# Kernel tuning notes

Hardware: AMD Instinct MI355X
Metric: run time of the kernel (lower is better)

Reference implementation:

```python
import jax, jax.numpy as jnp
import numpy as np


def setup_inputs() -> dict:
    key = jax.random.key(0)
    k_x, k_w, k_W, k_b, k_idx = jax.random.split(key, 5)
    B, C, N, K, O = 2, 32, 40962, 25, 64
    x = jax.random.normal(k_x, (B, C, N), dtype=jnp.float32)
    neigh_weights = jax.random.uniform(k_w, (N, K, 3), dtype=jnp.float32)
    W = jax.random.normal(k_W, (O, K * C), dtype=jnp.float32) * 0.02
    b = jax.random.normal(k_b, (O,), dtype=jnp.float32) * 0.02
    neigh_indices = jax.random.randint(k_idx, (N, K, 3), 0, N, dtype=jnp.int32)
    return {"x": x, "neigh_weights": neigh_weights, "W": W, "b": b,
            "neigh_indices": neigh_indices}


def reference(x, neigh_weights, W, b, neigh_indices):
    # x: (B, C, N); neigh_indices/neigh_weights: (N, K, 3); W: (O, C*K); b: (O,)
    B, C, N = x.shape
    _, K, _ = neigh_indices.shape
    # Gather neighbor features: (B, C, N, K, 3)
    mat = x[:, :, neigh_indices]
    # Barycentric weighted sum over the 3 triangle vertices -> (B, C, N, K)
    s = jnp.einsum('bcnkt,nkt->bcnk', mat, neigh_weights)
    # Permute to (B, N, C, K) and apply Linear(C*K -> O)
    feat = s.transpose(0, 2, 1, 3).reshape(B * N, C * K)
    out = feat @ W.T + b  # (B*N, O)
    out = out.reshape(B, N, -1).transpose(0, 2, 1)  # (B, O, N)
    return out
```

## Files before the change

kernel.cpp:

```cpp
#include <hip/hip_runtime.h>
#include <hip/hip_fp16.h>

typedef __attribute__((ext_vector_type(8))) _Float16 half8;
typedef __attribute__((ext_vector_type(4))) float f32x4;

union U2H2 { unsigned int u; __half2 h; };

static __device__ __forceinline__ unsigned int pack2h(float a, float b) {
    U2H2 c; c.h = __floats2half2_rn(a, b); return c.u;
}
static __device__ __forceinline__ __half2 u_as_h2(unsigned int u) {
    U2H2 c; c.u = u; return c.h;
}

#define SWZ(row, slot) ((slot) ^ ((row) & 3) ^ (((row) >> 2) & 3))

#define LDS_BARRIER()                                                \
    do {                                                             \
        asm volatile("s_waitcnt lgkmcnt(0)" ::: "memory");           \
        __builtin_amdgcn_s_barrier();                                \
        __builtin_amdgcn_sched_barrier(0);                           \
    } while (0)

__global__ void prep_w(const float* __restrict__ W, unsigned short* __restrict__ Wrh) {
    int i = blockIdx.x * 256 + threadIdx.x;
    if (i >= 25 * 2048) return;
    int c = i & 31, o = (i >> 5) & 63, k = i >> 11;
    __half h = __float2half(W[o * 800 + c * 25 + k]);
    Wrh[i] = *reinterpret_cast<unsigned short*>(&h);
}

__global__ __launch_bounds__(256) void transpose_x(const float* __restrict__ x,
                                                   unsigned short* __restrict__ xth, int N) {
    __shared__ float t[2][32][65];
    int n0 = blockIdx.x * 64, tid = threadIdx.x;
#pragma unroll
    for (int i = 0; i < 16; ++i) {
        int e = tid + 256 * i;
        int b = e >> 11, c = (e >> 6) & 31, nl = e & 63;
        int n = n0 + nl;
        t[b][c][nl] = (n < N) ? x[(size_t)(b * 32 + c) * N + n] : 0.f;
    }
    __syncthreads();
    int nl = tid >> 2, q = tid & 3, n = n0 + nl;
    if (n < N) {
#pragma unroll
        for (int b = 0; b < 2; ++b) {
            uint4 p;
            p.x = pack2h(t[b][q * 8 + 0][nl], t[b][q * 8 + 1][nl]);
            p.y = pack2h(t[b][q * 8 + 2][nl], t[b][q * 8 + 3][nl]);
            p.z = pack2h(t[b][q * 8 + 4][nl], t[b][q * 8 + 5][nl]);
            p.w = pack2h(t[b][q * 8 + 6][nl], t[b][q * 8 + 7][nl]);
            *reinterpret_cast<uint4*>(xth + ((size_t)n * 64 + b * 32 + q * 8)) = p;
        }
    }
}

__global__ __launch_bounds__(256) void fused_main(
    const unsigned short* __restrict__ xth,
    const unsigned short* __restrict__ Wrh,
    const float* __restrict__ bias,
    const int* __restrict__ nidx,
    const float* __restrict__ nw,
    float* __restrict__ out,
    int N)
{
    __shared__ unsigned int idxw[25 * 96];
    __shared__ __align__(16) unsigned char sA[2][4096];
    __shared__ __align__(16) unsigned char sB[2][4096];

    const int tid = threadIdx.x;
    const int n0 = blockIdx.x * 32;

#pragma unroll
    for (int it = 0; it < 10; ++it) {
        int e = tid + 256 * it;
        if (e < 2400) {
            int nl = e / 75;
            int rem = e - nl * 75;
            int n = n0 + nl;
            unsigned int u = 0;
            if (n < N) {
                int j = nidx[(size_t)n0 * 75 + e];
                __half hw = __float2half(nw[(size_t)n0 * 75 + e]);
                u = (unsigned int)j |
                    ((unsigned int)*reinterpret_cast<unsigned short*>(&hw) << 16);
            }
            int kk = rem / 3, t = rem - kk * 3;
            idxw[(kk * 32 + nl) * 3 + t] = u;
        }
    }
    __syncthreads();

    const int row = tid >> 2;
    const int l4  = tid & 3;
    const int b0  = row >> 5;
    const int nl0 = row & 31;

    const int wr_off = row * 64 + (SWZ(row, l4) << 4);
    const int sb_off = wr_off;

    const int l = tid & 63, wv = tid >> 6, c16 = l & 15, g = l >> 4;
    const int arow = 16 * wv + c16;
    const int rd_a = arow * 64 + (SWZ(arow, g) << 4);

    unsigned int ru[2][3];
    uint4 rg[2][3];
    uint4 rB;

    auto issue_g = [&](int kk, int buf) {
        const unsigned int* ip = &idxw[(kk * 32 + nl0) * 3];
#pragma unroll
        for (int t = 0; t < 3; ++t) {
            unsigned int u = ip[t];
            if (buf == 0) ru[0][t] = u; else ru[1][t] = u;
            uint4 v = *reinterpret_cast<const uint4*>(
                xth + ((size_t)(u & 0xffffu) * 64 + b0 * 32 + l4 * 8));
            if (buf == 0) rg[0][t] = v; else rg[1][t] = v;
        }
    };

    f32x4 acc[4];
#pragma unroll
    for (int ot = 0; ot < 4; ++ot) acc[ot] = (f32x4){0.f, 0.f, 0.f, 0.f};

    rB = *reinterpret_cast<const uint4*>(Wrh + tid * 8);
    issue_g(0, 0);
    issue_g(1, 1);

#pragma unroll 2
    for (int k = 0; k < 25; ++k) {
        const int buf = k & 1;

        *reinterpret_cast<uint4*>(&sB[buf][sb_off]) = rB;
        {
            int kB = (k + 1 < 25) ? k + 1 : 24;
            rB = *reinterpret_cast<const uint4*>(Wrh + kB * 2048 + tid * 8);
        }

        {
            unsigned int u0, u1, u2;
            uint4 v0, v1, v2;
            if (buf == 0) { u0 = ru[0][0]; u1 = ru[0][1]; u2 = ru[0][2];
                            v0 = rg[0][0]; v1 = rg[0][1]; v2 = rg[0][2]; }
            else          { u0 = ru[1][0]; u1 = ru[1][1]; u2 = ru[1][2];
                            v0 = rg[1][0]; v1 = rg[1][1]; v2 = rg[1][2]; }
            __half2 w0 = u_as_h2(__builtin_amdgcn_perm(u0, u0, 0x03020302u));
            __half2 w1 = u_as_h2(__builtin_amdgcn_perm(u1, u1, 0x03020302u));
            __half2 w2 = u_as_h2(__builtin_amdgcn_perm(u2, u2, 0x03020302u));
            uint4 p; U2H2 c;
            c.h = __hfma2(u_as_h2(v0.x), w0, __hfma2(u_as_h2(v1.x), w1, __hmul2(u_as_h2(v2.x), w2)));
            p.x = c.u;
            c.h = __hfma2(u_as_h2(v0.y), w0, __hfma2(u_as_h2(v1.y), w1, __hmul2(u_as_h2(v2.y), w2)));
            p.y = c.u;
            c.h = __hfma2(u_as_h2(v0.z), w0, __hfma2(u_as_h2(v1.z), w1, __hmul2(u_as_h2(v2.z), w2)));
            p.z = c.u;
            c.h = __hfma2(u_as_h2(v0.w), w0, __hfma2(u_as_h2(v1.w), w1, __hmul2(u_as_h2(v2.w), w2)));
            p.w = c.u;
            *reinterpret_cast<uint4*>(&sA[buf][wr_off]) = p;
        }
        {
            int kg = (k + 2 < 25) ? k + 2 : 24;
            issue_g(kg, buf);
        }

        LDS_BARRIER();

        {
            half8 af = *reinterpret_cast<const half8*>(&sA[buf][rd_a]);
#pragma unroll
            for (int ot = 0; ot < 4; ++ot) {
                int orow = ot * 16 + c16;
                half8 bf = *reinterpret_cast<const half8*>(
                    &sB[buf][orow * 64 + (SWZ(orow, g) << 4)]);
                acc[ot] = __builtin_amdgcn_mfma_f32_16x16x32_f16(af, bf, acc[ot], 0, 0, 0);
            }
        }
    }

#pragma unroll
    for (int ot = 0; ot < 4; ++ot) {
        int o = ot * 16 + c16;
        float bv = bias[o];
#pragma unroll
        for (int i = 0; i < 4; ++i) {
            int mrow = 16 * wv + 4 * g + i;
            int b = mrow >> 5, nl = mrow & 31;
            int n = n0 + nl;
            if (n < N) out[(size_t)(b * 64 + o) * N + n] = acc[ot][i] + bv;
        }
    }
}

extern "C" void kernel_launch(void* const* d_in, const int* in_sizes, int n_in,
                              void* d_out, int out_size, void* d_ws, size_t ws_size,
                              hipStream_t stream) {
    const float* x    = (const float*)d_in[0];
    const float* nw   = (const float*)d_in[1];
    const float* W    = (const float*)d_in[2];
    const float* bias = (const float*)d_in[3];
    const int*   nidx = (const int*)d_in[4];
    float* out = (float*)d_out;

    int N = in_sizes[0] / 64;

    unsigned short* xth = (unsigned short*)d_ws;
    unsigned short* Wrh = xth + (size_t)N * 64;

    prep_w<<<(25 * 2048 + 255) / 256, 256, 0, stream>>>(W, Wrh);

    transpose_x<<<(N + 63) / 64, 256, 0, stream>>>(x, xth, N);

    fused_main<<<(N + 31) / 32, 256, 0, stream>>>(xth, Wrh, bias, nidx, nw, out, N);
}
```

Before: 65.34 us.

## Feed MFMA operands directly from registers, removing LDS staging and barriers

Weights are pre-permuted into the MFMA B-fragment layout so each lane loads its own B operands straight from global memory. Each lane now gathers and blends the A fragment it needs itself, so the shared-memory sA/sB buffers and the per-iteration barrier go away. The loop is unrolled into explicit A/B register double buffers, with setprio around the MFMAs and a launch-bounds occupancy hint. The cost is more global B loads per lane (four instead of one, served by cache) and higher register pressure.

```diff
diff --git a/kernel.cpp b/kernel.cpp
--- a/kernel.cpp
+++ b/kernel.cpp
@@ -13,19 +13,16 @@
     U2H2 c; c.u = u; return c.h;
 }
 
-#define SWZ(row, slot) ((slot) ^ ((row) & 3) ^ (((row) >> 2) & 3))
-
-#define LDS_BARRIER()                                                \
-    do {                                                             \
-        asm volatile("s_waitcnt lgkmcnt(0)" ::: "memory");           \
-        __builtin_amdgcn_s_barrier();                                \
-        __builtin_amdgcn_sched_barrier(0);                           \
-    } while (0)
-
 __global__ void prep_w(const float* __restrict__ W, unsigned short* __restrict__ Wrh) {
     int i = blockIdx.x * 256 + threadIdx.x;
     if (i >= 25 * 2048) return;
-    int c = i & 31, o = (i >> 5) & 63, k = i >> 11;
+    int k = i >> 11;
+    int r = i & 2047;
+    int ot = r >> 9;
+    int l = (r >> 3) & 63;
+    int e = i & 7;
+    int o = ot * 16 + (l & 15);
+    int c = (l >> 4) * 8 + e;
     __half h = __float2half(W[o * 800 + c * 25 + k]);
     Wrh[i] = *reinterpret_cast<unsigned short*>(&h);
 }
@@ -56,7 +53,7 @@
     }
 }
 
-__global__ __launch_bounds__(256) void fused_main(
+__global__ __launch_bounds__(256, 4) void fused_main(
     const unsigned short* __restrict__ xth,
     const unsigned short* __restrict__ Wrh,
     const float* __restrict__ bias,
@@ -66,8 +63,6 @@
     int N)
 {
     __shared__ unsigned int idxw[25 * 96];
-    __shared__ __align__(16) unsigned char sA[2][4096];
-    __shared__ __align__(16) unsigned char sB[2][4096];
 
     const int tid = threadIdx.x;
     const int n0 = blockIdx.x * 32;
@@ -92,91 +87,75 @@
     }
     __syncthreads();
 
-    const int row = tid >> 2;
-    const int l4  = tid & 3;
-    const int b0  = row >> 5;
-    const int nl0 = row & 31;
+    const int wv = tid >> 6, l = tid & 63;
+    const int c16 = l & 15, g = l >> 4;
+    const int row = 16 * wv + c16;
+    const int b0 = row >> 5, nl0 = row & 31;
+    const int xoff = b0 * 32 + g * 8;
 
-    const int wr_off = row * 64 + (SWZ(row, l4) << 4);
-    const int sb_off = wr_off;
+    uint4 rgA[3], rgB[3], rBA[4], rBB[4];
+    unsigned int ruA[3], ruB[3];
 
-    const int l = tid & 63, wv = tid >> 6, c16 = l & 15, g = l >> 4;
-    const int arow = 16 * wv + c16;
-    const int rd_a = arow * 64 + (SWZ(arow, g) << 4);
-
-    unsigned int ru[2][3];
-    uint4 rg[2][3];
-    uint4 rB;
-
-    auto issue_g = [&](int kk, int buf) {
+    auto issue_g = [&](int kk, uint4 (&rg)[3], unsigned int (&ru)[3]) {
         const unsigned int* ip = &idxw[(kk * 32 + nl0) * 3];
 #pragma unroll
         for (int t = 0; t < 3; ++t) {
             unsigned int u = ip[t];
-            if (buf == 0) ru[0][t] = u; else ru[1][t] = u;
-            uint4 v = *reinterpret_cast<const uint4*>(
-                xth + ((size_t)(u & 0xffffu) * 64 + b0 * 32 + l4 * 8));
-            if (buf == 0) rg[0][t] = v; else rg[1][t] = v;
+            ru[t] = u;
+            rg[t] = *reinterpret_cast<const uint4*>(
+                xth + (int)(u & 0xffffu) * 64 + xoff);
         }
+    };
+    auto issue_B = [&](int kk, uint4 (&rB)[4]) {
+        const unsigned short* bp = Wrh + kk * 2048 + l * 8;
+#pragma unroll
+        for (int ot = 0; ot < 4; ++ot)
+            rB[ot] = *reinterpret_cast<const uint4*>(bp + ot * 512);
     };
 
     f32x4 acc[4];
 #pragma unroll
     for (int ot = 0; ot < 4; ++ot) acc[ot] = (f32x4){0.f, 0.f, 0.f, 0.f};
 
-    rB = *reinterpret_cast<const uint4*>(Wrh + tid * 8);
-    issue_g(0, 0);
-    issue_g(1, 1);
+    issue_g(0, rgA, ruA); issue_B(0, rBA);
+    issue_g(1, rgB, ruB); issue_B(1, rBB);
 
-#pragma unroll 2
-    for (int k = 0; k < 25; ++k) {
-        const int buf = k & 1;
+    auto body = [&](int kNext, uint4 (&rg)[3], unsigned int (&ru)[3], uint4 (&rB)[4]) {
+        __half2 w0 = u_as_h2(__builtin_amdgcn_perm(ru[0], ru[0], 0x03020302u));
+        __half2 w1 = u_as_h2(__builtin_amdgcn_perm(ru[1], ru[1], 0x03020302u));
+        __half2 w2 = u_as_h2(__builtin_amdgcn_perm(ru[2], ru[2], 0x03020302u));
+        uint4 v0 = rg[0], v1 = rg[1], v2 = rg[2];
+        uint4 p; U2H2 c;
+        c.h = __hfma2(u_as_h2(v0.x), w0, __hfma2(u_as_h2(v1.x), w1, __hmul2(u_as_h2(v2.x), w2)));
+        p.x = c.u;
+        c.h = __hfma2(u_as_h2(v0.y), w0, __hfma2(u_as_h2(v1.y), w1, __hmul2(u_as_h2(v2.y), w2)));
+        p.y = c.u;
+        c.h = __hfma2(u_as_h2(v0.z), w0, __hfma2(u_as_h2(v1.z), w1, __hmul2(u_as_h2(v2.z), w2)));
+        p.z = c.u;
+        c.h = __hfma2(u_as_h2(v0.w), w0, __hfma2(u_as_h2(v1.w), w1, __hmul2(u_as_h2(v2.w), w2)));
+        p.w = c.u;
+        half8 af = __builtin_bit_cast(half8, p);
 
-        *reinterpret_cast<uint4*>(&sB[buf][sb_off]) = rB;
-        {
-            int kB = (k + 1 < 25) ? k + 1 : 24;
-            rB = *reinterpret_cast<const uint4*>(Wrh + kB * 2048 + tid * 8);
+        issue_g(kNext, rg, ru);
+
+        __builtin_amdgcn_s_setprio(1);
+#pragma unroll
+        for (int ot = 0; ot < 4; ++ot) {
+            half8 bf = __builtin_bit_cast(half8, rB[ot]);
+            acc[ot] = __builtin_amdgcn_mfma_f32_16x16x32_f16(af, bf, acc[ot], 0, 0, 0);
         }
+        __builtin_amdgcn_s_setprio(0);
 
-        {
-            unsigned int u0, u1, u2;
-            uint4 v0, v1, v2;
-            if (buf == 0) { u0 = ru[0][0]; u1 = ru[0][1]; u2 = ru[0][2];
-                            v0 = rg[0][0]; v1 = rg[0][1]; v2 = rg[0][2]; }
-            else          { u0 = ru[1][0]; u1 = ru[1][1]; u2 = ru[1][2];
-                            v0 = rg[1][0]; v1 = rg[1][1]; v2 = rg[1][2]; }
-            __half2 w0 = u_as_h2(__builtin_amdgcn_perm(u0, u0, 0x03020302u));
-            __half2 w1 = u_as_h2(__builtin_amdgcn_perm(u1, u1, 0x03020302u));
-            __half2 w2 = u_as_h2(__builtin_amdgcn_perm(u2, u2, 0x03020302u));
-            uint4 p; U2H2 c;
-            c.h = __hfma2(u_as_h2(v0.x), w0, __hfma2(u_as_h2(v1.x), w1, __hmul2(u_as_h2(v2.x), w2)));
-            p.x = c.u;
-            c.h = __hfma2(u_as_h2(v0.y), w0, __hfma2(u_as_h2(v1.y), w1, __hmul2(u_as_h2(v2.y), w2)));
-            p.y = c.u;
-            c.h = __hfma2(u_as_h2(v0.z), w0, __hfma2(u_as_h2(v1.z), w1, __hmul2(u_as_h2(v2.z), w2)));
-            p.z = c.u;
-            c.h = __hfma2(u_as_h2(v0.w), w0, __hfma2(u_as_h2(v1.w), w1, __hmul2(u_as_h2(v2.w), w2)));
-            p.w = c.u;
-            *reinterpret_cast<uint4*>(&sA[buf][wr_off]) = p;
-        }
-        {
-            int kg = (k + 2 < 25) ? k + 2 : 24;
-            issue_g(kg, buf);
-        }
+        issue_B(kNext, rB);
+    };
 
-        LDS_BARRIER();
-
-        {
-            half8 af = *reinterpret_cast<const half8*>(&sA[buf][rd_a]);
-#pragma unroll
-            for (int ot = 0; ot < 4; ++ot) {
-                int orow = ot * 16 + c16;
-                half8 bf = *reinterpret_cast<const half8*>(
-                    &sB[buf][orow * 64 + (SWZ(orow, g) << 4)]);
-                acc[ot] = __builtin_amdgcn_mfma_f32_16x16x32_f16(af, bf, acc[ot], 0, 0, 0);
-            }
-        }
+    for (int kp = 0; kp < 12; ++kp) {
+        int kE = 2 * kp + 2;
+        int kO = (2 * kp + 3 <= 24) ? 2 * kp + 3 : 24;
+        body(kE, rgA, ruA, rBA);
+        body(kO, rgB, ruB, rBB);
     }
+    body(24, rgA, ruA, rBA);
 
 #pragma unroll
     for (int ot = 0; ot < 4; ++ot) {
```

Result: slower. 94.14 us (+44.1%).

## Deepen gather prefetch to four stages, merge prep kernels, simplify index staging

Applied to the files above, without the earlier changes.

Merges the weight-conversion and x-transpose prep kernels into one launch, with extra blocks handling the W conversion, which removes one kernel launch. In the main kernel, the neighbor-feature gather prefetch goes from two steps ahead to four, using four explicit register sets and a manually unrolled K loop, to hide more gather latency. The index/weight staging now stores in natural order (row*75), so the div/mod remapping goes away, and gather addressing uses 32-bit arithmetic. The trade-off is more live registers, which may reduce occupancy.

```diff
diff --git a/kernel.cpp b/kernel.cpp
--- a/kernel.cpp
+++ b/kernel.cpp
@@ -22,18 +22,25 @@
         __builtin_amdgcn_sched_barrier(0);                           \
     } while (0)
 
-__global__ void prep_w(const float* __restrict__ W, unsigned short* __restrict__ Wrh) {
-    int i = blockIdx.x * 256 + threadIdx.x;
-    if (i >= 25 * 2048) return;
-    int c = i & 31, o = (i >> 5) & 63, k = i >> 11;
-    __half h = __float2half(W[o * 800 + c * 25 + k]);
-    Wrh[i] = *reinterpret_cast<unsigned short*>(&h);
-}
-
-__global__ __launch_bounds__(256) void transpose_x(const float* __restrict__ x,
-                                                   unsigned short* __restrict__ xth, int N) {
+__global__ __launch_bounds__(256) void prep_all(const float* __restrict__ x,
+                                                const float* __restrict__ W,
+                                                unsigned short* __restrict__ xth,
+                                                unsigned short* __restrict__ Wrh,
+                                                int N, int nT) {
+    int bid = blockIdx.x, tid = threadIdx.x;
+    if (bid >= nT) {
+        int k = bid - nT;
+#pragma unroll
+        for (int it = 0; it < 8; ++it) {
+            int r = tid + 256 * it;
+            int o = r >> 5, c = r & 31;
+            __half h = __float2half(W[o * 800 + c * 25 + k]);
+            Wrh[k * 2048 + r] = *reinterpret_cast<unsigned short*>(&h);
+        }
+        return;
+    }
     __shared__ float t[2][32][65];
-    int n0 = blockIdx.x * 64, tid = threadIdx.x;
+    int n0 = bid * 64;
 #pragma unroll
     for (int i = 0; i < 16; ++i) {
         int e = tid + 256 * i;
@@ -65,7 +72,7 @@
     float* __restrict__ out,
     int N)
 {
-    __shared__ unsigned int idxw[25 * 96];
+    __shared__ unsigned int idxw[32 * 75];
     __shared__ __align__(16) unsigned char sA[2][4096];
     __shared__ __align__(16) unsigned char sB[2][4096];
 
@@ -76,9 +83,7 @@
     for (int it = 0; it < 10; ++it) {
         int e = tid + 256 * it;
         if (e < 2400) {
-            int nl = e / 75;
-            int rem = e - nl * 75;
-            int n = n0 + nl;
+            int n = n0 + e / 75;
             unsigned int u = 0;
             if (n < N) {
                 int j = nidx[(size_t)n0 * 75 + e];
@@ -86,8 +91,7 @@
                 u = (unsigned int)j |
                     ((unsigned int)*reinterpret_cast<unsigned short*>(&hw) << 16);
             }
-            int kk = rem / 3, t = rem - kk * 3;
-            idxw[(kk * 32 + nl) * 3 + t] = u;
+            idxw[e] = u;
         }
     }
     __syncthreads();
@@ -98,85 +102,92 @@
     const int nl0 = row & 31;
 
     const int wr_off = row * 64 + (SWZ(row, l4) << 4);
-    const int sb_off = wr_off;
 
     const int l = tid & 63, wv = tid >> 6, c16 = l & 15, g = l >> 4;
     const int arow = 16 * wv + c16;
     const int rd_a = arow * 64 + (SWZ(arow, g) << 4);
 
-    unsigned int ru[2][3];
-    uint4 rg[2][3];
+    uint4 rg0[3], rg1[3], rg2[3], rg3[3];
+    unsigned int ru0[3], ru1[3], ru2[3], ru3[3];
     uint4 rB;
 
-    auto issue_g = [&](int kk, int buf) {
-        const unsigned int* ip = &idxw[(kk * 32 + nl0) * 3];
-#pragma unroll
-        for (int t = 0; t < 3; ++t) {
-            unsigned int u = ip[t];
-            if (buf == 0) ru[0][t] = u; else ru[1][t] = u;
-            uint4 v = *reinterpret_cast<const uint4*>(
-                xth + ((size_t)(u & 0xffffu) * 64 + b0 * 32 + l4 * 8));
-            if (buf == 0) rg[0][t] = v; else rg[1][t] = v;
-        }
-    };
+    const unsigned int* iprow = &idxw[nl0 * 75];
+
+#define ISSUE_G(kk, RG, RU)                                                     \
+    do {                                                                        \
+        _Pragma("unroll")                                                       \
+        for (int t = 0; t < 3; ++t) {                                           \
+            unsigned int u = iprow[(kk) * 3 + t];                               \
+            RU[t] = u;                                                          \
+            RG[t] = *reinterpret_cast<const uint4*>(                            \
+                xth + (int)(u & 0xffffu) * 64 + b0 * 32 + l4 * 8);              \
+        }                                                                       \
+    } while (0)
 
     f32x4 acc[4];
 #pragma unroll
     for (int ot = 0; ot < 4; ++ot) acc[ot] = (f32x4){0.f, 0.f, 0.f, 0.f};
 
     rB = *reinterpret_cast<const uint4*>(Wrh + tid * 8);
-    issue_g(0, 0);
-    issue_g(1, 1);
-
-#pragma unroll 2
-    for (int k = 0; k < 25; ++k) {
-        const int buf = k & 1;
-
-        *reinterpret_cast<uint4*>(&sB[buf][sb_off]) = rB;
-        {
-            int kB = (k + 1 < 25) ? k + 1 : 24;
-            rB = *reinterpret_cast<const uint4*>(Wrh + kB * 2048 + tid * 8);
-        }
-
-        {
-            unsigned int u0, u1, u2;
-            uint4 v0, v1, v2;
-            if (buf == 0) { u0 = ru[0][0]; u1 = ru[0][1]; u2 = ru[0][2];
-                            v0 = rg[0][0]; v1 = rg[0][1]; v2 = rg[0][2]; }
-            else          { u0 = ru[1][0]; u1 = ru[1][1]; u2 = ru[1][2];
-                            v0 = rg[1][0]; v1 = rg[1][1]; v2 = rg[1][2]; }
-            __half2 w0 = u_as_h2(__builtin_amdgcn_perm(u0, u0, 0x03020302u));
-            __half2 w1 = u_as_h2(__builtin_amdgcn_perm(u1, u1, 0x03020302u));
-            __half2 w2 = u_as_h2(__builtin_amdgcn_perm(u2, u2, 0x03020302u));
-            uint4 p; U2H2 c;
-            c.h = __hfma2(u_as_h2(v0.x), w0, __hfma2(u_as_h2(v1.x), w1, __hmul2(u_as_h2(v2.x), w2)));
-            p.x = c.u;
-            c.h = __hfma2(u_as_h2(v0.y), w0, __hfma2(u_as_h2(v1.y), w1, __hmul2(u_as_h2(v2.y), w2)));
-            p.y = c.u;
-            c.h = __hfma2(u_as_h2(v0.z), w0, __hfma2(u_as_h2(v1.z), w1, __hmul2(u_as_h2(v2.z), w2)));
-            p.z = c.u;
-            c.h = __hfma2(u_as_h2(v0.w), w0, __hfma2(u_as_h2(v1.w), w1, __hmul2(u_as_h2(v2.w), w2)));
-            p.w = c.u;
-            *reinterpret_cast<uint4*>(&sA[buf][wr_off]) = p;
-        }
-        {
-            int kg = (k + 2 < 25) ? k + 2 : 24;
-            issue_g(kg, buf);
-        }
-
-        LDS_BARRIER();
-
-        {
-            half8 af = *reinterpret_cast<const half8*>(&sA[buf][rd_a]);
-#pragma unroll
-            for (int ot = 0; ot < 4; ++ot) {
-                int orow = ot * 16 + c16;
-                half8 bf = *reinterpret_cast<const half8*>(
-                    &sB[buf][orow * 64 + (SWZ(orow, g) << 4)]);
-                acc[ot] = __builtin_amdgcn_mfma_f32_16x16x32_f16(af, bf, acc[ot], 0, 0, 0);
-            }
-        }
-    }
+    ISSUE_G(0, rg0, ru0);
+    ISSUE_G(1, rg1, ru1);
+    ISSUE_G(2, rg2, ru2);
+    ISSUE_G(3, rg3, ru3);
+
+#define BODY(K, BUF, RG, RU)                                                       \
+    do {                                                                           \
+        const int k_ = (K);                                                        \
+                                              \
+        *reinterpret_cast<uint4*>(&sB[BUF][wr_off]) = rB;                          \
+        if (k_ + 1 < 25)                                                           \
+            rB = *reinterpret_cast<const uint4*>(Wrh + (k_ + 1) * 2048 + tid * 8); \
+                                   \
+        {                                                                          \
+            __half2 w0 = u_as_h2(__builtin_amdgcn_perm(RU[0], RU[0], 0x03020302u));\
+            __half2 w1 = u_as_h2(__builtin_amdgcn_perm(RU[1], RU[1], 0x03020302u));\
+            __half2 w2 = u_as_h2(__builtin_amdgcn_perm(RU[2], RU[2], 0x03020302u));\
+            uint4 v0 = RG[0], v1 = RG[1], v2 = RG[2];                              \
+            uint4 p; U2H2 c;                                                       \
+            c.h = __hfma2(u_as_h2(v0.x), w0,                                       \
+                  __hfma2(u_as_h2(v1.x), w1, __hmul2(u_as_h2(v2.x), w2)));         \
+            p.x = c.u;                                                             \
+            c.h = __hfma2(u_as_h2(v0.y), w0,                                       \
+                  __hfma2(u_as_h2(v1.y), w1, __hmul2(u_as_h2(v2.y), w2)));         \
+            p.y = c.u;                                                             \
+            c.h = __hfma2(u_as_h2(v0.z), w0,                                       \
+                  __hfma2(u_as_h2(v1.z), w1, __hmul2(u_as_h2(v2.z), w2)));         \
+            p.z = c.u;                                                             \
+            c.h = __hfma2(u_as_h2(v0.w), w0,                                       \
+                  __hfma2(u_as_h2(v1.w), w1, __hmul2(u_as_h2(v2.w), w2)));         \
+            p.w = c.u;                                                             \
+            *reinterpret_cast<uint4*>(&sA[BUF][wr_off]) = p;                       \
+        }                                                                          \
+                                     \
+        if (k_ + 4 < 25) ISSUE_G(k_ + 4, RG, RU);                                  \
+                      \
+        LDS_BARRIER();                                                             \
+                                                                \
+        {                                                                          \
+            half8 af = *reinterpret_cast<const half8*>(&sA[BUF][rd_a]);            \
+            _Pragma("unroll")                                                      \
+            for (int ot = 0; ot < 4; ++ot) {                                       \
+                int orow = ot * 16 + c16;                                          \
+                half8 bf = *reinterpret_cast<const half8*>(                        \
+                    &sB[BUF][orow * 64 + (SWZ(orow, g) << 4)]);                    \
+                acc[ot] =                                                          \
+                    __builtin_amdgcn_mfma_f32_16x16x32_f16(af, bf, acc[ot], 0, 0, 0);\
+            }                                                                      \
+        }                                                                          \
+    } while (0)
+
+    for (int kp = 0; kp < 6; ++kp) {
+        int k0 = kp * 4;
+        BODY(k0 + 0, 0, rg0, ru0);
+        BODY(k0 + 1, 1, rg1, ru1);
+        BODY(k0 + 2, 0, rg2, ru2);
+        BODY(k0 + 3, 1, rg3, ru3);
+    }
+    BODY(24, 0, rg0, ru0);
 
 #pragma unroll
     for (int ot = 0; ot < 4; ++ot) {
@@ -190,6 +201,8 @@
             if (n < N) out[(size_t)(b * 64 + o) * N + n] = acc[ot][i] + bv;
         }
     }
+#undef BODY
+#undef ISSUE_G
 }
 
 extern "C" void kernel_launch(void* const* d_in, const int* in_sizes, int n_in,
@@ -207,9 +220,8 @@
     unsigned short* xth = (unsigned short*)d_ws;
     unsigned short* Wrh = xth + (size_t)N * 64;
 
-    prep_w<<<(25 * 2048 + 255) / 256, 256, 0, stream>>>(W, Wrh);
-
-    transpose_x<<<(N + 63) / 64, 256, 0, stream>>>(x, xth, N);
+    int nT = (N + 63) / 64;
+    prep_all<<<nT + 25, 256, 0, stream>>>(x, W, xth, Wrh, N, nT);
 
     fused_main<<<(N + 31) / 32, 256, 0, stream>>>(xth, Wrh, bias, nidx, nw, out, N);
 }
```

After: 63.06 us. 3.5% less time.
